# Kernel optimization log

Measured on AMD Instinct MI355X. Metric: run time of the kernel, lower is better.

Reference implementation:

```python
import jax, jax.numpy as jnp
import numpy as np

OUT = 7   # output_size
SR = 2    # sampling_ratio
SCALES = (0.25, 0.125, 0.0625, 0.03125)  # inferred from feat sizes vs 800x800 image
K_MIN, LVL0, S0, EPS = 2, 4.0, 224.0, 1e-6


def _bilinear_gather(feat, b, y, x):
    """Legacy (aligned=False) bilinear sampling. feat [B,C,H,W]; b,y,x same shape S.
    Returns [*S, C]."""
    B, C, H, W = feat.shape
    valid = (y >= -1.0) & (y <= H) & (x >= -1.0) & (x <= W)
    y = jnp.maximum(y, 0.0)
    x = jnp.maximum(x, 0.0)
    yl = y.astype(jnp.int32)
    xl = x.astype(jnp.int32)
    ycond = yl >= H - 1
    yl = jnp.where(ycond, H - 1, yl)
    yh = jnp.where(ycond, H - 1, yl + 1)
    y = jnp.where(ycond, yl.astype(y.dtype), y)
    xcond = xl >= W - 1
    xl = jnp.where(xcond, W - 1, xl)
    xh = jnp.where(xcond, W - 1, xl + 1)
    x = jnp.where(xcond, xl.astype(x.dtype), x)
    ly = y - yl
    lx = x - xl
    hy = 1.0 - ly
    hx = 1.0 - lx
    def g(yy, xx):
        return feat[b, :, yy, xx]  # advanced indexing -> [*S, C]
    val = ((hy * hx)[..., None] * g(yl, xl)
           + (hy * lx)[..., None] * g(yl, xh)
           + (ly * hx)[..., None] * g(yh, xl)
           + (ly * lx)[..., None] * g(yh, xh))
    return jnp.where(valid[..., None], val, 0.0)


def _roi_align(feat, bidx, boxes, scale):
    """RoIAlign (aligned=False). feat [B,C,H,W], bidx [R] int, boxes [R,4] image coords.
    Returns [R,C,OUT,OUT]."""
    x1 = boxes[:, 0] * scale
    y1 = boxes[:, 1] * scale
    x2 = boxes[:, 2] * scale
    y2 = boxes[:, 3] * scale
    roi_w = jnp.maximum(x2 - x1, 1.0)
    roi_h = jnp.maximum(y2 - y1, 1.0)
    bin_h = roi_h / OUT
    bin_w = roi_w / OUT
    off = (jnp.arange(SR, dtype=feat.dtype) + 0.5) / SR      # [SR]
    ph = jnp.arange(OUT, dtype=feat.dtype)                   # [OUT]
    grid = ph[None, :, None] + off[None, None, :]            # [1,OUT,SR]
    ys = y1[:, None, None] + grid * bin_h[:, None, None]     # [R,OUT,SR]
    xs = x1[:, None, None] + grid * bin_w[:, None, None]     # [R,OUT,SR]
    Y = ys[:, :, None, :, None]                              # [R,OUT,1,SR,1]
    X = xs[:, None, :, None, :]                              # [R,1,OUT,1,SR]
    Yb, Xb = jnp.broadcast_arrays(Y, X)                      # [R,OUT,OUT,SR,SR]
    b = jnp.broadcast_to(bidx[:, None, None, None, None], Yb.shape)
    val = _bilinear_gather(feat, b, Yb, Xb)                  # [R,OUT,OUT,SR,SR,C]
    pooled = val.mean(axis=(3, 4))                           # [R,OUT,OUT,C]
    return jnp.transpose(pooled, (0, 3, 1, 2))               # [R,C,OUT,OUT]


def _levels(boxes_flat):
    """LevelMapper.run: FPN level index (0-based) per RoI."""
    area = (boxes_flat[:, 2] - boxes_flat[:, 0]) * (boxes_flat[:, 3] - boxes_flat[:, 1])
    s = jnp.sqrt(area)
    lvl = jnp.floor(LVL0 + jnp.log2(s / S0 + EPS))
    return jnp.clip(lvl, K_MIN, K_MIN + 3).astype(jnp.int32) - K_MIN


def setup_inputs() -> dict:
    key = jax.random.key(0)
    ks = jax.random.split(key, 6)
    sizes = [200, 100, 50, 25]
    inp = {f"feat{i}": jax.random.normal(ks[i], (2, 256, s, s), dtype=jnp.float32)
           for i, s in enumerate(sizes)}
    xy = jax.random.uniform(ks[4], (2, 256, 2), dtype=jnp.float32) * 500.0
    wh = jax.random.uniform(ks[5], (2, 256, 2), dtype=jnp.float32) * 400.0 + 8.0
    inp["boxes"] = jnp.concatenate([xy, xy + wh], axis=-1)  # (x1,y1,x2,y2) in [0,908)
    return inp


def reference(feat0, feat1, feat2, feat3, boxes):
    feats = [feat0, feat1, feat2, feat3]
    B, N, _ = boxes.shape
    bf = boxes.reshape(B * N, 4)
    bidx = jnp.repeat(jnp.arange(B, dtype=jnp.int32), N)  # convert_to_roi_format ids
    lv = _levels(bf)
    C = feats[0].shape[1]
    out = jnp.zeros((B * N, C, OUT, OUT), dtype=feats[0].dtype)
    for level, (f, sc) in enumerate(zip(feats, SCALES)):
        r = _roi_align(f, bidx, bf, sc)
        out = jnp.where((lv == level)[:, None, None, None], r, out)
    return out
```

## Files before the change

### kernel.cpp

```cpp
#include <hip/hip_runtime.h>

#define OUT 7
#define NCH 256
#define NB 2
#define NPER 256
#define NROI (NB * NPER)
#define TPR (NCH * OUT * OUT)
#define BPR (TPR / 256)

__device__ __forceinline__ float rfl_f(float v) {
    return __int_as_float(__builtin_amdgcn_readfirstlane(__float_as_int(v)));
}

__global__ __launch_bounds__(256) void roi_align_kernel(
        const float* __restrict__ f0, const float* __restrict__ f1,
        const float* __restrict__ f2, const float* __restrict__ f3,
        const float* __restrict__ boxes, float* __restrict__ out) {
    int b    = blockIdx.x;
    int xcd  = b & 7;
    int slot = b >> 3;
    int rr   = slot / BPR;
    int j    = slot - rr * BPR;
    int r    = (rr << 3) | xcd;

    int lin = j * 256 + (int)threadIdx.x;
    int pw  = lin % OUT;
    int t   = lin / OUT;
    int ph  = t % OUT;
    int c   = t / OUT;

    float bx1 = rfl_f(boxes[r * 4 + 0]);
    float by1 = rfl_f(boxes[r * 4 + 1]);
    float bx2 = rfl_f(boxes[r * 4 + 2]);
    float by2 = rfl_f(boxes[r * 4 + 3]);

    float area = (bx2 - bx1) * (by2 - by1);
    float s    = sqrtf(area);
    float lvl  = floorf(4.0f + log2f(s * (1.0f / 224.0f) + 1e-6f));
    lvl        = fminf(fmaxf(lvl, 2.0f), 5.0f);
    int level  = __builtin_amdgcn_readfirstlane((int)lvl - 2);

    const float* f;
    int H;
    float scale;
    switch (level) {
        case 0:  f = f0; H = 200; scale = 0.25f;    break;
        case 1:  f = f1; H = 100; scale = 0.125f;   break;
        case 2:  f = f2; H = 50;  scale = 0.0625f;  break;
        default: f = f3; H = 25;  scale = 0.03125f; break;
    }
    float Hf = (float)H;

    float x1 = bx1 * scale;
    float y1 = by1 * scale;
    float roi_w = fmaxf(bx2 * scale - x1, 1.0f);
    float roi_h = fmaxf(by2 * scale - y1, 1.0f);
    float bin_w = roi_w * (1.0f / OUT);
    float bin_h = roi_h * (1.0f / OUT);

    int bidx = r >> 8;
    const float* plane = f + (size_t)(bidx * NCH + c) * (size_t)(H * H);

    float wgt[16];
    int   off[16];
#pragma unroll
    for (int iy = 0; iy < 2; ++iy) {
        float y   = y1 + ((float)ph + (iy ? 0.75f : 0.25f)) * bin_h;
        bool  oky = (y >= -1.0f) && (y <= Hf);
        y = fmaxf(y, 0.0f);
        int yl = (int)y;
        int yh;
        if (yl >= H - 1) { yl = H - 1; yh = H - 1; y = (float)yl; }
        else             { yh = yl + 1; }
        float ly = y - (float)yl;
        float hy = 1.0f - ly;
        int rl = yl * H;
        int rh = yh * H;
#pragma unroll
        for (int ix = 0; ix < 2; ++ix) {
            float x  = x1 + ((float)pw + (ix ? 0.75f : 0.25f)) * bin_w;
            bool  ok = oky && (x >= -1.0f) && (x <= Hf);
            x = fmaxf(x, 0.0f);
            int xl = (int)x;
            int xh;
            if (xl >= H - 1) { xl = H - 1; xh = H - 1; x = (float)xl; }
            else             { xh = xl + 1; }
            float lx = x - (float)xl;
            float hx = 1.0f - lx;
            float m  = ok ? 0.25f : 0.0f;
            int k = (iy * 2 + ix) * 4;
            wgt[k + 0] = hy * hx * m;  off[k + 0] = rl + xl;
            wgt[k + 1] = hy * lx * m;  off[k + 1] = rl + xh;
            wgt[k + 2] = ly * hx * m;  off[k + 2] = rh + xl;
            wgt[k + 3] = ly * lx * m;  off[k + 3] = rh + xh;
        }
    }

    float v[16];
#pragma unroll
    for (int k = 0; k < 16; ++k) v[k] = plane[off[k]];

    float acc = 0.0f;
#pragma unroll
    for (int k = 0; k < 16; ++k) acc = fmaf(wgt[k], v[k], acc);

    out[(size_t)r * TPR + lin] = acc;
}

extern "C" void kernel_launch(void* const* d_in, const int* in_sizes, int n_in,
                              void* d_out, int out_size, void* d_ws, size_t ws_size,
                              hipStream_t stream) {
    const float* f0    = (const float*)d_in[0];
    const float* f1    = (const float*)d_in[1];
    const float* f2    = (const float*)d_in[2];
    const float* f3    = (const float*)d_in[3];
    const float* boxes = (const float*)d_in[4];
    float* out         = (float*)d_out;

    const int grid = NROI * BPR;
    roi_align_kernel<<<grid, 256, 0, stream>>>(f0, f1, f2, f3, boxes, out);
}
```

Before: 203.4 us.

## Transpose feature maps to channels-last bf16 workspace before RoIAlign gather

Adds per-level transpose kernels that turn the NCHW fp32 feature maps into channels-last bf16 in the workspace. A new RoIAlign kernel then gathers, for each sample point, 64 contiguous channels per wave and stages results in LDS for coalesced output writes. The aim is to replace the scattered per-channel-plane gathers with coalesced channel-contiguous loads at half the bytes. In exchange it transposes every feature map each call, which adds about 27 MB of extra reads and writes, and bf16 storage loses precision against the fp32 reference. The old direct kernel is kept as a fallback when the workspace is too small.

Measured after the change: 226.5 us. 1.11x slower.

```diff
diff --git a/kernel.cpp b/kernel.cpp
--- a/kernel.cpp
+++ b/kernel.cpp
@@ -6,21 +6,166 @@
 #define NPER 256
 #define NROI (NB * NPER)
 #define TPR (NCH * OUT * OUT)
-#define BPR (TPR / 256)
+
+#define P0 (200 * 200)
+#define P1 (100 * 100)
+#define P2 (50 * 50)
+#define P3 (25 * 25)
+#define BASE0 0
+#define BASE1 (BASE0 + NB * P0 * NCH)
+#define BASE2 (BASE1 + NB * P1 * NCH)
+#define BASE3 (BASE2 + NB * P2 * NCH)
+#define WS_ELEMS (BASE3 + NB * P3 * NCH)
 
 __device__ __forceinline__ float rfl_f(float v) {
     return __int_as_float(__builtin_amdgcn_readfirstlane(__float_as_int(v)));
 }
 
-__global__ __launch_bounds__(256) void roi_align_kernel(
+__device__ __forceinline__ unsigned short f2bf_rne(float f) {
+    unsigned int u = __float_as_uint(f);
+    u += 0x7FFFu + ((u >> 16) & 1u);
+    return (unsigned short)(u >> 16);
+}
+
+__device__ __forceinline__ float bf2f(unsigned short h) {
+    return __uint_as_float((unsigned int)h << 16);
+}
+
+__global__ __launch_bounds__(256) void transpose_cl_kernel(
+        const float* __restrict__ src, unsigned short* __restrict__ dst, int P) {
+    __shared__ float tile[64][65];
+    int p0 = blockIdx.x * 64;
+    int c0 = blockIdx.y * 64;
+    int b  = blockIdx.z;
+    int tx = threadIdx.x & 63;
+    int ty = threadIdx.x >> 6;
+
+#pragma unroll
+    for (int k = 0; k < 16; ++k) {
+        int cc = ty + 4 * k;
+        int p  = p0 + tx;
+        float v = (p < P) ? src[((size_t)(b * NCH + c0 + cc)) * P + p] : 0.0f;
+        tile[cc][tx] = v;
+    }
+    __syncthreads();
+#pragma unroll
+    for (int k = 0; k < 16; ++k) {
+        int pp = ty + 4 * k;
+        int p  = p0 + pp;
+        if (p < P)
+            dst[((size_t)b * P + p) * NCH + c0 + tx] = f2bf_rne(tile[tx][pp]);
+    }
+}
+
+__global__ __launch_bounds__(256) void roi_align_cl_kernel(
+        const unsigned short* __restrict__ t,
+        const float* __restrict__ boxes, float* __restrict__ out) {
+    __shared__ float lds[64 * 49];
+    int blk  = blockIdx.x;
+    int r    = blk >> 2;
+    int q    = blk & 3;
+    int lane = threadIdx.x & 63;
+    int wave = threadIdx.x >> 6;
+
+    float bx1 = rfl_f(boxes[r * 4 + 0]);
+    float by1 = rfl_f(boxes[r * 4 + 1]);
+    float bx2 = rfl_f(boxes[r * 4 + 2]);
+    float by2 = rfl_f(boxes[r * 4 + 3]);
+
+    float area = (bx2 - bx1) * (by2 - by1);
+    float s    = sqrtf(area);
+    float lvl  = floorf(4.0f + log2f(s * (1.0f / 224.0f) + 1e-6f));
+    lvl        = fminf(fmaxf(lvl, 2.0f), 5.0f);
+    int level  = __builtin_amdgcn_readfirstlane((int)lvl - 2);
+
+    int H; float scale; size_t base;
+    switch (level) {
+        case 0:  H = 200; scale = 0.25f;    base = BASE0; break;
+        case 1:  H = 100; scale = 0.125f;   base = BASE1; break;
+        case 2:  H = 50;  scale = 0.0625f;  base = BASE2; break;
+        default: H = 25;  scale = 0.03125f; base = BASE3; break;
+    }
+    float Hf = (float)H;
+
+    float x1 = bx1 * scale;
+    float y1 = by1 * scale;
+    float roi_w = fmaxf(bx2 * scale - x1, 1.0f);
+    float roi_h = fmaxf(by2 * scale - y1, 1.0f);
+    float bin_w = roi_w * (1.0f / OUT);
+    float bin_h = roi_h * (1.0f / OUT);
+
+    int bidx = r >> 8;
+    const unsigned short* plane =
+        t + base + (size_t)bidx * (size_t)(H * H) * NCH + (size_t)(q * 64 + lane);
+
+    for (int p = wave; p < OUT * OUT; p += 4) {
+        int ph = p / OUT;
+        int pw = p - ph * OUT;
+
+        float wgt[16];
+        int   off[16];
+#pragma unroll
+        for (int iy = 0; iy < 2; ++iy) {
+            float y   = y1 + ((float)ph + (iy ? 0.75f : 0.25f)) * bin_h;
+            bool  oky = (y >= -1.0f) && (y <= Hf);
+            y = fmaxf(y, 0.0f);
+            int yl = (int)y;
+            int yh;
+            if (yl >= H - 1) { yl = H - 1; yh = H - 1; y = (float)yl; }
+            else             { yh = yl + 1; }
+            float ly = y - (float)yl;
+            float hy = 1.0f - ly;
+            int rl = yl * H;
+            int rh = yh * H;
+#pragma unroll
+            for (int ix = 0; ix < 2; ++ix) {
+                float x  = x1 + ((float)pw + (ix ? 0.75f : 0.25f)) * bin_w;
+                bool  ok = oky && (x >= -1.0f) && (x <= Hf);
+                x = fmaxf(x, 0.0f);
+                int xl = (int)x;
+                int xh;
+                if (xl >= H - 1) { xl = H - 1; xh = H - 1; x = (float)xl; }
+                else             { xh = xl + 1; }
+                float lx = x - (float)xl;
+                float hx = 1.0f - lx;
+                float m  = ok ? 0.25f : 0.0f;
+                int k = (iy * 2 + ix) * 4;
+                wgt[k + 0] = hy * hx * m;  off[k + 0] = (rl + xl) * NCH;
+                wgt[k + 1] = hy * lx * m;  off[k + 1] = (rl + xh) * NCH;
+                wgt[k + 2] = ly * hx * m;  off[k + 2] = (rh + xl) * NCH;
+                wgt[k + 3] = ly * lx * m;  off[k + 3] = (rh + xh) * NCH;
+            }
+        }
+
+        unsigned short v[16];
+#pragma unroll
+        for (int k = 0; k < 16; ++k) v[k] = plane[off[k]];
+
+        float acc = 0.0f;
+#pragma unroll
+        for (int k = 0; k < 16; ++k) acc = fmaf(wgt[k], bf2f(v[k]), acc);
+
+        lds[lane * 49 + p] = acc;
+    }
+    __syncthreads();
+
+    float* dst = out + (size_t)r * TPR + (size_t)q * 3136;
+    for (int e = threadIdx.x; e < 3136; e += 256) {
+        int c_l = e / 49;
+        int p   = e - c_l * 49;
+        dst[e] = lds[c_l * 49 + p];
+    }
+}
+
+__global__ __launch_bounds__(256) void roi_align_direct_kernel(
         const float* __restrict__ f0, const float* __restrict__ f1,
         const float* __restrict__ f2, const float* __restrict__ f3,
         const float* __restrict__ boxes, float* __restrict__ out) {
     int b    = blockIdx.x;
     int xcd  = b & 7;
     int slot = b >> 3;
-    int rr   = slot / BPR;
-    int j    = slot - rr * BPR;
+    int rr   = slot / 49;
+    int j    = slot - rr * 49;
     int r    = (rr << 3) | xcd;
 
     int lin = j * 256 + (int)threadIdx.x;
@@ -117,6 +262,14 @@
     const float* boxes = (const float*)d_in[4];
     float* out         = (float*)d_out;
 
-    const int grid = NROI * BPR;
-    roi_align_kernel<<<grid, 256, 0, stream>>>(f0, f1, f2, f3, boxes, out);
-}
+    if (ws_size >= (size_t)WS_ELEMS * sizeof(unsigned short)) {
+        unsigned short* t = (unsigned short*)d_ws;
+        transpose_cl_kernel<<<dim3((P0 + 63) / 64, 4, NB), 256, 0, stream>>>(f0, t + BASE0, P0);
+        transpose_cl_kernel<<<dim3((P1 + 63) / 64, 4, NB), 256, 0, stream>>>(f1, t + BASE1, P1);
+        transpose_cl_kernel<<<dim3((P2 + 63) / 64, 4, NB), 256, 0, stream>>>(f2, t + BASE2, P2);
+        transpose_cl_kernel<<<dim3((P3 + 63) / 64, 4, NB), 256, 0, stream>>>(f3, t + BASE3, P3);
+        roi_align_cl_kernel<<<NROI * 4, 256, 0, stream>>>(t, boxes, out);
+    } else {
+        roi_align_direct_kernel<<<NROI * 49, 256, 0, stream>>>(f0, f1, f2, f3, boxes, out);
+    }
+}
```

## Stage deduplicated bilinear taps in LDS as bf16 per ROI channel chunk

Applied to the files above, without the earlier changes.

Each block now handles one ROI and 32 channels. It first computes the 28 row and 28 column tap indices and weights once per ROI. It then gathers the 28x28 tap grid for those channels into shared memory as bf16, so duplicated taps are fetched only once, and does the bilinear accumulation from LDS with two channels packed per word. Results are transposed through LDS so the global stores are coalesced. Converting to bf16 loses precision and could break tolerance, and the scattered global gather loop may still limit throughput.

Measured after the change: 245.7 us. +20.8%, slower.

```diff
diff --git a/kernel.cpp b/kernel.cpp
--- a/kernel.cpp
+++ b/kernel.cpp
@@ -2,32 +2,36 @@
 
 #define OUT 7
 #define NCH 256
-#define NB 2
-#define NPER 256
-#define NROI (NB * NPER)
+#define NROI 512
+#define NS 14
+#define NT 28
+#define CCH 32
+#define CPAD 34
 #define TPR (NCH * OUT * OUT)
-#define BPR (TPR / 256)
 
 __device__ __forceinline__ float rfl_f(float v) {
     return __int_as_float(__builtin_amdgcn_readfirstlane(__float_as_int(v)));
 }
 
-__global__ __launch_bounds__(256) void roi_align_kernel(
+__device__ __forceinline__ unsigned short f2bf_rne(float f) {
+    unsigned int u = __float_as_uint(f);
+    u += 0x7FFFu + ((u >> 16) & 1u);
+    return (unsigned short)(u >> 16);
+}
+
+__global__ __launch_bounds__(256, 3) void roi_align_tap_kernel(
         const float* __restrict__ f0, const float* __restrict__ f1,
         const float* __restrict__ f2, const float* __restrict__ f3,
         const float* __restrict__ boxes, float* __restrict__ out) {
-    int b    = blockIdx.x;
-    int xcd  = b & 7;
-    int slot = b >> 3;
-    int rr   = slot / BPR;
-    int j    = slot - rr * BPR;
-    int r    = (rr << 3) | xcd;
+    __shared__ unsigned short sm[NT * NT * CPAD];
+    __shared__ int   rowIdx[NT];
+    __shared__ int   colIdx[NT];
+    __shared__ float lyS[NS], vyS[NS], lxS[NS], vxS[NS];
 
-    int lin = j * 256 + (int)threadIdx.x;
-    int pw  = lin % OUT;
-    int t   = lin / OUT;
-    int ph  = t % OUT;
-    int c   = t / OUT;
+    int blk = blockIdx.x;
+    int r   = blk >> 3;
+    int q   = blk & 7;
+    int tid = (int)threadIdx.x;
 
     float bx1 = rfl_f(boxes[r * 4 + 0]);
     float by1 = rfl_f(boxes[r * 4 + 1]);
@@ -40,9 +44,7 @@
     lvl        = fminf(fmaxf(lvl, 2.0f), 5.0f);
     int level  = __builtin_amdgcn_readfirstlane((int)lvl - 2);
 
-    const float* f;
-    int H;
-    float scale;
+    const float* f; int H; float scale;
     switch (level) {
         case 0:  f = f0; H = 200; scale = 0.25f;    break;
         case 1:  f = f1; H = 100; scale = 0.125f;   break;
@@ -51,60 +53,126 @@
     }
     float Hf = (float)H;
 
-    float x1 = bx1 * scale;
-    float y1 = by1 * scale;
+    float x1 = bx1 * scale, y1 = by1 * scale;
     float roi_w = fmaxf(bx2 * scale - x1, 1.0f);
     float roi_h = fmaxf(by2 * scale - y1, 1.0f);
     float bin_w = roi_w * (1.0f / OUT);
     float bin_h = roi_h * (1.0f / OUT);
 
+    if (tid < NS) {
+        int ph = tid >> 1, iy = tid & 1;
+        float y = y1 + ((float)ph + (iy ? 0.75f : 0.25f)) * bin_h;
+        float v = (y >= -1.0f && y <= Hf) ? 0.5f : 0.0f;
+        y = fmaxf(y, 0.0f);
+        int yl = (int)y, yh;
+        float ly;
+        if (yl >= H - 1) { yl = H - 1; yh = H - 1; ly = 0.0f; }
+        else             { yh = yl + 1; ly = y - (float)yl; }
+        lyS[tid] = ly; vyS[tid] = v;
+        rowIdx[2 * tid]     = yl;
+        rowIdx[2 * tid + 1] = yh;
+    } else if (tid >= 32 && tid < 32 + NS) {
+        int t = tid - 32;
+        int pw = t >> 1, ix = t & 1;
+        float x = x1 + ((float)pw + (ix ? 0.75f : 0.25f)) * bin_w;
+        float v = (x >= -1.0f && x <= Hf) ? 0.5f : 0.0f;
+        x = fmaxf(x, 0.0f);
+        int xl = (int)x, xh;
+        float lx;
+        if (xl >= H - 1) { xl = H - 1; xh = H - 1; lx = 0.0f; }
+        else             { xh = xl + 1; lx = x - (float)xl; }
+        lxS[t] = lx; vxS[t] = v;
+        colIdx[2 * t]     = xl;
+        colIdx[2 * t + 1] = xh;
+    }
+    __syncthreads();
+
     int bidx = r >> 8;
-    const float* plane = f + (size_t)(bidx * NCH + c) * (size_t)(H * H);
+    const float* plane = f + (size_t)(bidx * NCH + q * CCH) * (size_t)(H * H);
+    size_t HH = (size_t)(H * H);
 
-    float wgt[16];
-    int   off[16];
+    int lane = tid & 63;
+    int wave = tid >> 6;
+    int j    = lane & 31;
+    int ch2  = lane >> 5;
+    bool jok = (j < NT);
+    int col  = jok ? colIdx[j] : 0;
+
 #pragma unroll
-    for (int iy = 0; iy < 2; ++iy) {
-        float y   = y1 + ((float)ph + (iy ? 0.75f : 0.25f)) * bin_h;
-        bool  oky = (y >= -1.0f) && (y <= Hf);
-        y = fmaxf(y, 0.0f);
-        int yl = (int)y;
-        int yh;
-        if (yl >= H - 1) { yl = H - 1; yh = H - 1; y = (float)yl; }
-        else             { yh = yl + 1; }
-        float ly = y - (float)yl;
-        float hy = 1.0f - ly;
-        int rl = yl * H;
-        int rh = yh * H;
-#pragma unroll
-        for (int ix = 0; ix < 2; ++ix) {
-            float x  = x1 + ((float)pw + (ix ? 0.75f : 0.25f)) * bin_w;
-            bool  ok = oky && (x >= -1.0f) && (x <= Hf);
-            x = fmaxf(x, 0.0f);
-            int xl = (int)x;
-            int xh;
-            if (xl >= H - 1) { xl = H - 1; xh = H - 1; x = (float)xl; }
-            else             { xh = xl + 1; }
-            float lx = x - (float)xl;
-            float hx = 1.0f - lx;
-            float m  = ok ? 0.25f : 0.0f;
-            int k = (iy * 2 + ix) * 4;
-            wgt[k + 0] = hy * hx * m;  off[k + 0] = rl + xl;
-            wgt[k + 1] = hy * lx * m;  off[k + 1] = rl + xh;
-            wgt[k + 2] = ly * hx * m;  off[k + 2] = rh + xl;
-            wgt[k + 3] = ly * lx * m;  off[k + 3] = rh + xh;
+    for (int t = 0; t < 7; ++t) {
+        int i = wave * 7 + t;
+        size_t rbase = (size_t)rowIdx[i] * (size_t)H + (size_t)col;
+        unsigned short* smrow = sm + (i * NT + j) * CPAD;
+#pragma unroll 4
+        for (int cc = 0; cc < 16; ++cc) {
+            int ch = ch2 * 16 + cc;
+            float v = 0.0f;
+            if (jok) v = plane[(size_t)ch * HH + rbase];
+            if (jok) smrow[ch] = f2bf_rne(v);
         }
     }
+    __syncthreads();
 
-    float v[16];
+    const unsigned int* smw = (const unsigned int*)sm;
+    float accx[4], accy[4];
 #pragma unroll
-    for (int k = 0; k < 16; ++k) v[k] = plane[off[k]];
+    for (int i = 0; i < 4; ++i) { accx[i] = 0.0f; accy[i] = 0.0f; }
 
-    float acc = 0.0f;
 #pragma unroll
-    for (int k = 0; k < 16; ++k) acc = fmaf(wgt[k], v[k], acc);
+    for (int i = 0; i < 4; ++i) {
+        int o = tid + 256 * i;
+        if (o < 784) {
+            int px = o >> 4, cp = o & 15;
+            int ph = px / 7, pw = px - ph * 7;
+            float ax = 0.0f, ay = 0.0f;
+#pragma unroll
+            for (int iy = 0; iy < 2; ++iy) {
+                int sy = ph * 2 + iy;
+                float ly = lyS[sy], hy = 1.0f - ly;
+                float vy = vyS[sy];
+                int r0 = (2 * sy) * NT;
+                int r1 = (2 * sy + 1) * NT;
+#pragma unroll
+                for (int ix = 0; ix < 2; ++ix) {
+                    int sx = pw * 2 + ix;
+                    float lx = lxS[sx], hx = 1.0f - lx;
+                    float m  = vy * vxS[sx];
+                    int c0 = 2 * sx, c1 = 2 * sx + 1;
+                    unsigned int u00 = smw[(r0 + c0) * 17 + cp];
+                    unsigned int u01 = smw[(r0 + c1) * 17 + cp];
+                    unsigned int u10 = smw[(r1 + c0) * 17 + cp];
+                    unsigned int u11 = smw[(r1 + c1) * 17 + cp];
+                    float w00 = hy * hx * m, w01 = hy * lx * m;
+                    float w10 = ly * hx * m, w11 = ly * lx * m;
+                    ax = fmaf(w00, __uint_as_float(u00 << 16), ax);
+                    ay = fmaf(w00, __uint_as_float(u00 & 0xFFFF0000u), ay);
+                    ax = fmaf(w01, __uint_as_float(u01 << 16), ax);
+                    ay = fmaf(w01, __uint_as_float(u01 & 0xFFFF0000u), ay);
+                    ax = fmaf(w10, __uint_as_float(u10 << 16), ax);
+                    ay = fmaf(w10, __uint_as_float(u10 & 0xFFFF0000u), ay);
+                    ax = fmaf(w11, __uint_as_float(u11 << 16), ax);
+                    ay = fmaf(w11, __uint_as_float(u11 & 0xFFFF0000u), ay);
+                }
+            }
+            accx[i] = ax; accy[i] = ay;
+        }
+    }
+    __syncthreads();
 
-    out[(size_t)r * TPR + lin] = acc;
+    float* smf = (float*)sm;
+#pragma unroll
+    for (int i = 0; i < 4; ++i) {
+        int o = tid + 256 * i;
+        if (o < 784) {
+            int px = o >> 4, cp = o & 15;
+            smf[(cp * 2 + 0) * 49 + px] = accx[i];
+            smf[(cp * 2 + 1) * 49 + px] = accy[i];
+        }
+    }
+    __syncthreads();
+
+    float* dst = out + (size_t)r * TPR + (size_t)q * (CCH * 49);
+    for (int e = tid; e < CCH * 49; e += 256) dst[e] = smf[e];
 }
 
 extern "C" void kernel_launch(void* const* d_in, const int* in_sizes, int n_in,
@@ -117,6 +185,5 @@
     const float* boxes = (const float*)d_in[4];
     float* out         = (float*)d_out;
 
-    const int grid = NROI * BPR;
-    roi_align_kernel<<<grid, 256, 0, stream>>>(f0, f1, f2, f3, boxes, out);
+    roi_align_tap_kernel<<<NROI * 8, 256, 0, stream>>>(f0, f1, f2, f3, boxes, out);
 }
```
